# Performance work log

Hardware: AMD Instinct MI355X
Metric: run time of the kernel (lower is better)

## Reference

```python
import jax, jax.numpy as jnp
import numpy as np

M, N1, N2, DX, H = 4, 1024, 1024, 3, 64


def setup_inputs() -> dict:
    key = jax.random.key(0)
    ks = jax.random.split(key, 8)
    diff = jax.random.normal(ks[0], (M, N1, N2, DX), dtype=jnp.float32)
    mask = jax.random.randint(ks[1], (M, N1, N2), 0, 2) == 1  # True -> masked out
    W1 = jax.random.normal(ks[2], (DX, H), dtype=jnp.float32) / np.float32(np.sqrt(DX))
    b1 = jnp.zeros((H,), jnp.float32)
    W2 = jax.random.normal(ks[3], (H, H), dtype=jnp.float32) / np.float32(np.sqrt(H))
    b2 = jnp.zeros((H,), jnp.float32)
    W3 = jax.random.normal(ks[4], (H, 1), dtype=jnp.float32) / np.float32(np.sqrt(H))
    b3 = jnp.zeros((1,), jnp.float32)
    return {"diff": diff, "mask": mask, "W1": W1, "b1": b1,
            "W2": W2, "b2": b2, "W3": W3, "b3": b3}


def reference(diff, mask, W1, b1, W2, b2, W3, b3):
    # MLP applied pointwise over [m, n1, n2, dx] -> scalar score per (m, n1, n2)
    h = jax.nn.relu(jnp.einsum("mijd,dh->mijh", diff, W1) + b1)
    h = jax.nn.relu(jnp.einsum("mijh,hk->mijk", h, W2) + b2)
    dots = (jnp.einsum("mijh,ho->mijo", h, W3) + b3)[..., 0]  # [m, n1, n2]
    # masked_fill(mask, -inf) then softmax over n2
    dots = jnp.where(mask, -jnp.inf, dots)
    return jax.nn.softmax(dots, axis=-1)
```

## Files before the change

### kernel.cpp

```cpp
#include <hip/hip_runtime.h>
#include <hip/hip_fp16.h>
#include <math.h>

typedef __attribute__((ext_vector_type(8))) _Float16 half8;
typedef __attribute__((ext_vector_type(2))) __fp16 fp16x2;
typedef __attribute__((ext_vector_type(4))) float float4v;
typedef __attribute__((ext_vector_type(2))) float float2v;

#define MFMA_F16 __builtin_amdgcn_mfma_f32_16x16x32_f16

__global__ __launch_bounds__(256, 2) void mlp_softmax_kernel(
    const float* __restrict__ diff, const int* __restrict__ mask,
    const float* __restrict__ W1, const float* __restrict__ b1,
    const float* __restrict__ W2, const float* __restrict__ b2,
    const float* __restrict__ W3, float* __restrict__ out)
{
    __shared__ float s_diff[3072];
    __shared__ float s_w2[4096];
    __shared__ float s_w1[192];
    __shared__ float s_b1[64];
    __shared__ float s_b2[64];
    __shared__ float s_w3[64];
    __shared__ float s_red[8];

    float* const s_dots = s_w2;

    const int tid = threadIdx.x;
    const int bid = blockIdx.x;
    const long row_off = (long)bid * 3072;

    {
        const float4v* gd = (const float4v*)(diff + row_off);
        float4v* sd = (float4v*)s_diff;
        #pragma unroll
        for (int it = 0; it < 3; ++it) sd[tid + 256 * it] = gd[tid + 256 * it];
        const float4v* gw2 = (const float4v*)W2;
        float4v* sw2 = (float4v*)s_w2;
        #pragma unroll
        for (int it = 0; it < 4; ++it) sw2[tid + 256 * it] = gw2[tid + 256 * it];
        if (tid < 48)                    ((float4v*)s_w1)[tid]      = ((const float4v*)W1)[tid];
        else if (tid >= 64 && tid < 80)  ((float4v*)s_b1)[tid - 64] = ((const float4v*)b1)[tid - 64];
        else if (tid >= 80 && tid < 96)  ((float4v*)s_b2)[tid - 80] = ((const float4v*)b2)[tid - 80];
        else if (tid >= 96 && tid < 112) ((float4v*)s_w3)[tid - 96] = ((const float4v*)W3)[tid - 96];
    }
    __syncthreads();

    const int lane = tid & 63;
    const int wv   = tid >> 6;
    const int lg   = lane >> 4;
    const int lr   = lane & 15;

    const int hb0 = lg * 8;
    float2v w1p[2][3][4], b1p[2][4];
    #pragma unroll
    for (int kh = 0; kh < 2; ++kh) {
        const int hb = kh * 32 + hb0;
        #pragma unroll
        for (int p = 0; p < 4; ++p) {
            b1p[kh][p] = *(const float2v*)&s_b1[hb + 2 * p];
            #pragma unroll
            for (int d = 0; d < 3; ++d)
                w1p[kh][d][p] = *(const float2v*)&s_w1[d * 64 + hb + 2 * p];
        }
    }
    half8 bfr[4][2];
    #pragma unroll
    for (int nt = 0; nt < 4; ++nt) {
        #pragma unroll
        for (int kh = 0; kh < 2; ++kh) {
            union { fp16x2 h2[4]; half8 h8; } u;
            #pragma unroll
            for (int ep = 0; ep < 4; ++ep) {
                const int k0 = kh * 32 + lg * 8 + ep * 2;
                const float f0 = s_w2[(k0    ) * 64 + nt * 16 + lr];
                const float f1 = s_w2[(k0 + 1) * 64 + nt * 16 + lr];
                u.h2[ep] = __builtin_amdgcn_cvt_pkrtz(f0, f1);
            }
            bfr[nt][kh] = u.h8;
        }
    }
    float4v b2v[4], w3v[4];
    #pragma unroll
    for (int nt = 0; nt < 4; ++nt) {
        b2v[nt] = *(const float4v*)&s_b2[nt * 16 + lg * 4];
        w3v[nt] = *(const float4v*)&s_w3[nt * 16 + lg * 4];
    }
    __syncthreads();

    const float2v zero2 = {0.0f, 0.0f};
    const float4v zero4 = {0.0f, 0.0f, 0.0f, 0.0f};

    const int jw0 = wv * 256;
    for (int t = 0; t < 16; ++t) {
        const int j0 = jw0 + t * 16;
        const int jp = j0 + lr;
        const float x0 = s_diff[jp * 3 + 0];
        const float x1 = s_diff[jp * 3 + 1];
        const float x2 = s_diff[jp * 3 + 2];
        const float2v x0p = {x0, x0}, x1p = {x1, x1}, x2p = {x2, x2};

        half8 afr[2];
        #pragma unroll
        for (int kh = 0; kh < 2; ++kh) {
            union { fp16x2 h2[4]; half8 h8; } u;
            #pragma unroll
            for (int p = 0; p < 4; ++p) {
                float2v h = b1p[kh][p];
                h = __builtin_elementwise_fma(x0p, w1p[kh][0][p], h);
                h = __builtin_elementwise_fma(x1p, w1p[kh][1][p], h);
                h = __builtin_elementwise_fma(x2p, w1p[kh][2][p], h);
                h = __builtin_elementwise_max(h, zero2);
                u.h2[p] = __builtin_amdgcn_cvt_pkrtz(h[0], h[1]);
            }
            afr[kh] = u.h8;
        }

        float2v sr2 = zero2;
        #pragma unroll
        for (int nt = 0; nt < 4; ++nt) {
            float4v acc = b2v[nt];
            acc = MFMA_F16(bfr[nt][0], afr[0], acc, 0, 0, 0);
            acc = MFMA_F16(bfr[nt][1], afr[1], acc, 0, 0, 0);
            const float4v rl = __builtin_elementwise_max(acc, zero4);
            const float2v rlo = {rl[0], rl[1]}, rhi = {rl[2], rl[3]};
            const float2v wlo = {w3v[nt][0], w3v[nt][1]};
            const float2v whi = {w3v[nt][2], w3v[nt][3]};
            sr2 = __builtin_elementwise_fma(rlo, wlo, sr2);
            sr2 = __builtin_elementwise_fma(rhi, whi, sr2);
        }
        float sr = sr2[0] + sr2[1];
        sr += __shfl_xor(sr, 16, 64);
        sr += __shfl_xor(sr, 32, 64);
        if (lane < 16) s_dots[j0 + lane] = sr;
    }
    __syncthreads();

    const int j4 = tid * 4;
    float4v dv = *(const float4v*)&s_dots[j4];
    const int4 mv = *(const int4*)(mask + (long)bid * 1024 + j4);
    const float NINF = -__builtin_inff();
    float d0 = mv.x ? NINF : dv[0];
    float d1 = mv.y ? NINF : dv[1];
    float d2 = mv.z ? NINF : dv[2];
    float d3 = mv.w ? NINF : dv[3];

    float mx = fmaxf(fmaxf(d0, d1), fmaxf(d2, d3));
    #pragma unroll
    for (int off = 1; off < 64; off <<= 1) mx = fmaxf(mx, __shfl_xor(mx, off, 64));
    if (lane == 0) s_red[wv] = mx;
    __syncthreads();
    mx = fmaxf(fmaxf(s_red[0], s_red[1]), fmaxf(s_red[2], s_red[3]));

    const float e0 = mv.x ? 0.0f : __expf(d0 - mx);
    const float e1 = mv.y ? 0.0f : __expf(d1 - mx);
    const float e2 = mv.z ? 0.0f : __expf(d2 - mx);
    const float e3 = mv.w ? 0.0f : __expf(d3 - mx);
    float s = (e0 + e1) + (e2 + e3);
    #pragma unroll
    for (int off = 1; off < 64; off <<= 1) s += __shfl_xor(s, off, 64);
    if (lane == 0) s_red[4 + wv] = s;
    __syncthreads();
    const float tot = (s_red[4] + s_red[5]) + (s_red[6] + s_red[7]);
    const float inv = 1.0f / tot;

    float4v ov = {e0 * inv, e1 * inv, e2 * inv, e3 * inv};
    *(float4v*)(out + (long)bid * 1024 + j4) = ov;
}

extern "C" void kernel_launch(void* const* d_in, const int* in_sizes, int n_in,
                              void* d_out, int out_size, void* d_ws, size_t ws_size,
                              hipStream_t stream) {
    const float* diff = (const float*)d_in[0];
    const int*   mask = (const int*)d_in[1];
    const float* W1   = (const float*)d_in[2];
    const float* b1   = (const float*)d_in[3];
    const float* W2   = (const float*)d_in[4];
    const float* b2   = (const float*)d_in[5];
    const float* W3   = (const float*)d_in[6];
    float* out = (float*)d_out;

    mlp_softmax_kernel<<<dim3(4096), dim3(256), 0, stream>>>(
        diff, mask, W1, b1, W2, b2, W3, out);
}
```

Measured before the change: 169.9 us.

## Prepack weights in a setup kernel and process one softmax row per wavefront

A tiny prepack kernel converts W2 into per-lane fp16 MFMA fragments and lays out W1, b1, b2 and W3 in workspace once per call. The main kernel now maps each wavefront to a full row, so a block covers four rows and the cross-wave shared-memory reductions and block barriers in the softmax go away. Diff is read straight from global memory instead of being staged through LDS, and occupancy is raised to four blocks per SM. The cost is an extra kernel launch, strided uncoalesced global loads of diff, and 16 scalar mask loads and output stores per lane instead of vector accesses.

```diff
diff --git a/kernel.cpp b/kernel.cpp
--- a/kernel.cpp
+++ b/kernel.cpp
@@ -9,61 +9,12 @@
 
 #define MFMA_F16 __builtin_amdgcn_mfma_f32_16x16x32_f16
 
-__global__ __launch_bounds__(256, 2) void mlp_softmax_kernel(
-    const float* __restrict__ diff, const int* __restrict__ mask,
-    const float* __restrict__ W1, const float* __restrict__ b1,
-    const float* __restrict__ W2, const float* __restrict__ b2,
-    const float* __restrict__ W3, float* __restrict__ out)
+__global__ void prepack_kernel(const float* __restrict__ W1, const float* __restrict__ b1,
+                               const float* __restrict__ W2, const float* __restrict__ b2,
+                               const float* __restrict__ W3, char* __restrict__ ws)
 {
-    __shared__ float s_diff[3072];
-    __shared__ float s_w2[4096];
-    __shared__ float s_w1[192];
-    __shared__ float s_b1[64];
-    __shared__ float s_b2[64];
-    __shared__ float s_w3[64];
-    __shared__ float s_red[8];
-
-    float* const s_dots = s_w2;
-
-    const int tid = threadIdx.x;
-    const int bid = blockIdx.x;
-    const long row_off = (long)bid * 3072;
-
-    {
-        const float4v* gd = (const float4v*)(diff + row_off);
-        float4v* sd = (float4v*)s_diff;
-        #pragma unroll
-        for (int it = 0; it < 3; ++it) sd[tid + 256 * it] = gd[tid + 256 * it];
-        const float4v* gw2 = (const float4v*)W2;
-        float4v* sw2 = (float4v*)s_w2;
-        #pragma unroll
-        for (int it = 0; it < 4; ++it) sw2[tid + 256 * it] = gw2[tid + 256 * it];
-        if (tid < 48)                    ((float4v*)s_w1)[tid]      = ((const float4v*)W1)[tid];
-        else if (tid >= 64 && tid < 80)  ((float4v*)s_b1)[tid - 64] = ((const float4v*)b1)[tid - 64];
-        else if (tid >= 80 && tid < 96)  ((float4v*)s_b2)[tid - 80] = ((const float4v*)b2)[tid - 80];
-        else if (tid >= 96 && tid < 112) ((float4v*)s_w3)[tid - 96] = ((const float4v*)W3)[tid - 96];
-    }
-    __syncthreads();
-
-    const int lane = tid & 63;
-    const int wv   = tid >> 6;
-    const int lg   = lane >> 4;
-    const int lr   = lane & 15;
-
-    const int hb0 = lg * 8;
-    float2v w1p[2][3][4], b1p[2][4];
-    #pragma unroll
-    for (int kh = 0; kh < 2; ++kh) {
-        const int hb = kh * 32 + hb0;
-        #pragma unroll
-        for (int p = 0; p < 4; ++p) {
-            b1p[kh][p] = *(const float2v*)&s_b1[hb + 2 * p];
-            #pragma unroll
-            for (int d = 0; d < 3; ++d)
-                w1p[kh][d][p] = *(const float2v*)&s_w1[d * 64 + hb + 2 * p];
-        }
-    }
-    half8 bfr[4][2];
+    const int lane = threadIdx.x & 63;
+    const int lg = lane >> 4, lr = lane & 15;
     #pragma unroll
     for (int nt = 0; nt < 4; ++nt) {
         #pragma unroll
@@ -72,31 +23,94 @@
             #pragma unroll
             for (int ep = 0; ep < 4; ++ep) {
                 const int k0 = kh * 32 + lg * 8 + ep * 2;
-                const float f0 = s_w2[(k0    ) * 64 + nt * 16 + lr];
-                const float f1 = s_w2[(k0 + 1) * 64 + nt * 16 + lr];
-                u.h2[ep] = __builtin_amdgcn_cvt_pkrtz(f0, f1);
+                u.h2[ep] = __builtin_amdgcn_cvt_pkrtz(W2[k0 * 64 + nt * 16 + lr],
+                                                      W2[(k0 + 1) * 64 + nt * 16 + lr]);
             }
-            bfr[nt][kh] = u.h8;
+            *(half8*)(ws + lane * 128 + nt * 32 + kh * 16) = u.h8;
         }
     }
+    if (lane < 4) {
+        char* base = ws + 8192 + lane * 256;
+        #pragma unroll
+        for (int kh = 0; kh < 2; ++kh) {
+            #pragma unroll
+            for (int p = 0; p < 4; ++p) {
+                const int h = kh * 32 + lane * 8 + 2 * p;
+                #pragma unroll
+                for (int d = 0; d < 3; ++d) {
+                    float2v w = {W1[d * 64 + h], W1[d * 64 + h + 1]};
+                    *(float2v*)(base + kh * 96 + d * 32 + p * 8) = w;
+                }
+                float2v bb = {b1[h], b1[h + 1]};
+                *(float2v*)(base + 192 + kh * 32 + p * 8) = bb;
+            }
+        }
+    } else if (lane >= 8 && lane < 12) {
+        const int lgx = lane - 8;
+        char* base = ws + 9216 + lgx * 128;
+        #pragma unroll
+        for (int nt = 0; nt < 4; ++nt) {
+            const int h0 = nt * 16 + lgx * 4;
+            float4v bv = {b2[h0], b2[h0 + 1], b2[h0 + 2], b2[h0 + 3]};
+            *(float4v*)(base + nt * 16) = bv;
+            float4v w3_ = {W3[h0], W3[h0 + 1], W3[h0 + 2], W3[h0 + 3]};
+            *(float4v*)(base + 64 + nt * 16) = w3_;
+        }
+    }
+}
+
+__global__ __launch_bounds__(256, 4) void mlp_softmax_kernel(
+    const float* __restrict__ diff, const int* __restrict__ mask,
+    const char* __restrict__ ws, float* __restrict__ out)
+{
+    __shared__ float s_dots[4][1024];
+    __shared__ char  s_tab[1536];
+
+    const int tid = threadIdx.x;
+    if (tid < 96) ((float4v*)s_tab)[tid] = ((const float4v*)(ws + 8192))[tid];
+    __syncthreads();
+
+    const int lane = tid & 63, wv = tid >> 6;
+    const int lg = lane >> 4,  lr = lane & 15;
+    const int row = blockIdx.x * 4 + wv;
+
+    half8 bfr[4][2];
+    #pragma unroll
+    for (int nt = 0; nt < 4; ++nt)
+        #pragma unroll
+        for (int kh = 0; kh < 2; ++kh)
+            bfr[nt][kh] = *(const half8*)(ws + lane * 128 + nt * 32 + kh * 16);
+
+    const char* tb = s_tab + lg * 256;
+    float2v w1p[2][3][4], b1p[2][4];
+    #pragma unroll
+    for (int kh = 0; kh < 2; ++kh) {
+        #pragma unroll
+        for (int p = 0; p < 4; ++p) {
+            #pragma unroll
+            for (int d = 0; d < 3; ++d)
+                w1p[kh][d][p] = *(const float2v*)(tb + kh * 96 + d * 32 + p * 8);
+            b1p[kh][p] = *(const float2v*)(tb + 192 + kh * 32 + p * 8);
+        }
+    }
+    const char* tc = s_tab + 1024 + lg * 128;
     float4v b2v[4], w3v[4];
     #pragma unroll
     for (int nt = 0; nt < 4; ++nt) {
-        b2v[nt] = *(const float4v*)&s_b2[nt * 16 + lg * 4];
-        w3v[nt] = *(const float4v*)&s_w3[nt * 16 + lg * 4];
+        b2v[nt] = *(const float4v*)(tc + nt * 16);
+        w3v[nt] = *(const float4v*)(tc + 64 + nt * 16);
     }
-    __syncthreads();
 
+    const float* drow = diff + (long)row * 3072;
     const float2v zero2 = {0.0f, 0.0f};
     const float4v zero4 = {0.0f, 0.0f, 0.0f, 0.0f};
 
-    const int jw0 = wv * 256;
-    for (int t = 0; t < 16; ++t) {
-        const int j0 = jw0 + t * 16;
-        const int jp = j0 + lr;
-        const float x0 = s_diff[jp * 3 + 0];
-        const float x1 = s_diff[jp * 3 + 1];
-        const float x2 = s_diff[jp * 3 + 2];
+    #pragma unroll 2
+    for (int t = 0; t < 64; ++t) {
+        const int jp = t * 16 + lr;
+        const float x0 = drow[jp * 3 + 0];
+        const float x1 = drow[jp * 3 + 1];
+        const float x2 = drow[jp * 3 + 2];
         const float2v x0p = {x0, x0}, x1p = {x1, x1}, x2p = {x2, x2};
 
         half8 afr[2];
@@ -131,40 +145,32 @@
         float sr = sr2[0] + sr2[1];
         sr += __shfl_xor(sr, 16, 64);
         sr += __shfl_xor(sr, 32, 64);
-        if (lane < 16) s_dots[j0 + lane] = sr;
+        if (lane < 16) s_dots[wv][t * 16 + lane] = sr;
     }
     __syncthreads();
 
-    const int j4 = tid * 4;
-    float4v dv = *(const float4v*)&s_dots[j4];
-    const int4 mv = *(const int4*)(mask + (long)bid * 1024 + j4);
-    const float NINF = -__builtin_inff();
-    float d0 = mv.x ? NINF : dv[0];
-    float d1 = mv.y ? NINF : dv[1];
-    float d2 = mv.z ? NINF : dv[2];
-    float d3 = mv.w ? NINF : dv[3];
-
-    float mx = fmaxf(fmaxf(d0, d1), fmaxf(d2, d3));
+    const int* mrow = mask + (long)row * 1024;
+    float d[16];
+    #pragma unroll
+    for (int i = 0; i < 16; ++i) {
+        const int p = lane + 64 * i;
+        const int mv = mrow[p];
+        d[i] = mv ? -__builtin_inff() : s_dots[wv][p];
+    }
+    float mx = d[0];
+    #pragma unroll
+    for (int i = 1; i < 16; ++i) mx = fmaxf(mx, d[i]);
     #pragma unroll
     for (int off = 1; off < 64; off <<= 1) mx = fmaxf(mx, __shfl_xor(mx, off, 64));
-    if (lane == 0) s_red[wv] = mx;
-    __syncthreads();
-    mx = fmaxf(fmaxf(s_red[0], s_red[1]), fmaxf(s_red[2], s_red[3]));
-
-    const float e0 = mv.x ? 0.0f : __expf(d0 - mx);
-    const float e1 = mv.y ? 0.0f : __expf(d1 - mx);
-    const float e2 = mv.z ? 0.0f : __expf(d2 - mx);
-    const float e3 = mv.w ? 0.0f : __expf(d3 - mx);
-    float s = (e0 + e1) + (e2 + e3);
+    float s = 0.0f;
+    #pragma unroll
+    for (int i = 0; i < 16; ++i) { d[i] = __expf(d[i] - mx); s += d[i]; }
     #pragma unroll
     for (int off = 1; off < 64; off <<= 1) s += __shfl_xor(s, off, 64);
-    if (lane == 0) s_red[4 + wv] = s;
-    __syncthreads();
-    const float tot = (s_red[4] + s_red[5]) + (s_red[6] + s_red[7]);
-    const float inv = 1.0f / tot;
-
-    float4v ov = {e0 * inv, e1 * inv, e2 * inv, e3 * inv};
-    *(float4v*)(out + (long)bid * 1024 + j4) = ov;
+    const float inv = 1.0f / s;
+    float* orow = out + (long)row * 1024;
+    #pragma unroll
+    for (int i = 0; i < 16; ++i) orow[lane + 64 * i] = d[i] * inv;
 }
 
 extern "C" void kernel_launch(void* const* d_in, const int* in_sizes, int n_in,
@@ -178,7 +184,8 @@
     const float* b2   = (const float*)d_in[5];
     const float* W3   = (const float*)d_in[6];
     float* out = (float*)d_out;
+    char*  ws  = (char*)d_ws;
 
-    mlp_softmax_kernel<<<dim3(4096), dim3(256), 0, stream>>>(
-        diff, mask, W1, b1, W2, b2, W3, out);
+    prepack_kernel<<<dim3(1), dim3(64), 0, stream>>>(W1, b1, W2, b2, W3, ws);
+    mlp_softmax_kernel<<<dim3(1024), dim3(256), 0, stream>>>(diff, mask, ws, out);
 }
```

Measured after the change: 324.9 us. +91.2%, slower.
